# Performance work log

Hardware: AMD Instinct MI355X
Metric: run time of the kernel (lower is better)

## Reference

```python
import jax, jax.numpy as jnp
import numpy as np

B, V, E, H, L = 1024, 50257, 512, 512, 2


def setup_inputs() -> dict:
    key = jax.random.key(0)
    ks = jax.random.split(key, 12)
    s = 1.0 / np.sqrt(H)
    inp = {
        "x": jax.random.randint(ks[0], (B,), 0, V),
        "hidden": jnp.zeros((2 * L, B, H), jnp.float32),
        "embed": jax.random.normal(ks[1], (V, E), jnp.float32) * 0.02,
        # layer 0: input size E; layer 1: input size 2H (bidirectional concat)
        "Wih0": jax.random.uniform(ks[2], (2, 3 * H, E), jnp.float32, -s, s),
        "Whh0": jax.random.uniform(ks[3], (2, 3 * H, H), jnp.float32, -s, s),
        "bih0": jax.random.uniform(ks[4], (2, 3 * H), jnp.float32, -s, s),
        "bhh0": jax.random.uniform(ks[5], (2, 3 * H), jnp.float32, -s, s),
        "Wih1": jax.random.uniform(ks[6], (2, 3 * H, 2 * H), jnp.float32, -s, s),
        "Whh1": jax.random.uniform(ks[7], (2, 3 * H, H), jnp.float32, -s, s),
        "bih1": jax.random.uniform(ks[8], (2, 3 * H), jnp.float32, -s, s),
        "bhh1": jax.random.uniform(ks[9], (2, 3 * H), jnp.float32, -s, s),
        "Wproj": jax.random.uniform(ks[10], (V, E), jnp.float32, -1.0 / np.sqrt(E), 1.0 / np.sqrt(E)),
        "bproj": jax.random.uniform(ks[11], (V,), jnp.float32, -1.0 / np.sqrt(E), 1.0 / np.sqrt(E)),
    }
    return inp


def _gru_cell(x, h, Wih, Whh, bih, bhh):
    # PyTorch GRU cell: gates ordered (r, z, n)
    gi = x @ Wih.T + bih            # [B, 3H]
    gh = h @ Whh.T + bhh            # [B, 3H]
    ir, iz, inn = jnp.split(gi, 3, axis=-1)
    hr, hz, hn = jnp.split(gh, 3, axis=-1)
    r = jax.nn.sigmoid(ir + hr)
    z = jax.nn.sigmoid(iz + hz)
    n = jnp.tanh(inn + r * hn)
    return (1.0 - z) * n + z * h


def reference(x, hidden, embed, Wih0, Whh0, bih0, bhh0, Wih1, Whh1, bih1, bhh1, Wproj, bproj):
    inp = embed[x]                  # [B, E] embedding lookup; seq_len == 1
    layer_params = [(Wih0, Whh0, bih0, bhh0), (Wih1, Whh1, bih1, bhh1)]
    new_h = []
    for l, (Wih, Whh, bih, bhh) in enumerate(layer_params):
        # single timestep: fwd and bwd directions each do one cell step on the same input
        hf = _gru_cell(inp, hidden[2 * l],     Wih[0], Whh[0], bih[0], bhh[0])
        hb = _gru_cell(inp, hidden[2 * l + 1], Wih[1], Whh[1], bih[1], bhh[1])
        new_h += [hf, hb]
        inp = jnp.concatenate([hf, hb], axis=-1)   # [B, 2H]
    # x[:, :, hidden_dim:] -> backward-direction output of top layer, then transpose(0,1)
    out = hb[:, None, :]                            # [B, 1, H]
    logits = out @ Wproj.T + bproj                  # [B, 1, V]
    probs = jax.nn.softmax(logits, axis=-1)
    return probs, jnp.stack(new_h, axis=0)          # ([B,1,V], [2L, B, H])
```

## Files before the change

kernel.cpp:

```cpp
#include <hip/hip_runtime.h>


#define Bsz 1024
#define Hs  512
#define Vv  50257
#define VP  50304
#define NG  1536
#define NPB 393

typedef __bf16 bf16x8 __attribute__((ext_vector_type(8)));
typedef float  floatx4 __attribute__((ext_vector_type(4)));

__device__ __forceinline__ unsigned short f2bf(float f) {
  unsigned int u = __builtin_bit_cast(unsigned int, f);
  u += 0x7fffu + ((u >> 16) & 1u);
  return (unsigned short)(u >> 16);
}

__device__ __forceinline__ float bf2f(unsigned short u) {
  unsigned int x = (unsigned int)u << 16;
  return __builtin_bit_cast(float, x);
}

__device__ __forceinline__ void cvt4(const float* src, unsigned short* dst) {
  float4 f = *(const float4*)src;
  unsigned int lo = (unsigned int)f2bf(f.x) | ((unsigned int)f2bf(f.y) << 16);
  unsigned int hi = (unsigned int)f2bf(f.z) | ((unsigned int)f2bf(f.w) << 16);
  *(uint2*)dst = make_uint2(lo, hi);
}

__device__ __forceinline__ void g2lds16(const void* g, void* l) {
  unsigned long long gv = (unsigned long long)g;
  unsigned int lv = (unsigned int)(unsigned long long)l;
  __builtin_amdgcn_global_load_lds(
      (const __attribute__((address_space(1))) unsigned int*)gv,
      (__attribute__((address_space(3))) unsigned int*)lv,
      16, 0, 0);
}

__device__ __forceinline__ void compute_step(const unsigned short* Acur, const unsigned short* Bcur,
                                             floatx4 (&acc)[4][4], int wr, int wc, int g, int r16) {
#pragma unroll
  for (int ks = 0; ks < 2; ++ks) {
    bf16x8 a[4], b[4];
#pragma unroll
    for (int i = 0; i < 4; ++i) {
      int rowA = wr * 64 + i * 16 + r16;
      int ca = (ks * 4 + g) ^ (rowA & 7);
      a[i] = *(const bf16x8*)((const char*)Acur + rowA * 128 + ca * 16);
      int rowB = wc * 64 + i * 16 + r16;
      int cb = (ks * 4 + g) ^ (rowB & 7);
      b[i] = *(const bf16x8*)((const char*)Bcur + rowB * 128 + cb * 16);
    }
#pragma unroll
    for (int i = 0; i < 4; ++i)
#pragma unroll
      for (int j = 0; j < 4; ++j)
        acc[i][j] = __builtin_amdgcn_mfma_f32_16x16x32_bf16(a[i], b[j], acc[i][j], 0, 0, 0);
  }
}

__device__ __forceinline__ void gemm_core8(const unsigned short* A, const unsigned short* Bw, int K,
                                           int mt, int nt,
                                           unsigned short* Alds, unsigned short* Blds,
                                           floatx4 (&acc)[4][4]) {
  const int tid = threadIdx.x;
  const int w = tid >> 6, l = tid & 63;
  const int wr = w >> 1, wc = w & 1;
  const int g = l >> 4, r16 = l & 15;
  floatx4 zero = {0.f, 0.f, 0.f, 0.f};
#pragma unroll
  for (int i = 0; i < 4; ++i)
#pragma unroll
    for (int j = 0; j < 4; ++j) acc[i][j] = zero;

  const int nsteps = K >> 6;
  for (int kt = 0; kt < nsteps; ++kt) {
    __syncthreads();
#pragma unroll
    for (int i = 0; i < 4; ++i) {
      int chunk = w * 4 + i;
      int t16 = chunk * 64 + l;
      int row = t16 >> 3, c = t16 & 7;
      int sc = c ^ (row & 7);
      g2lds16(A + (size_t)(mt * 256 + row) * K + kt * 64 + sc * 8, (char*)Alds + chunk * 1024);
    }
#pragma unroll
    for (int i = 0; i < 2; ++i) {
      int chunk = w * 2 + i;
      int t16 = chunk * 64 + l;
      int row = t16 >> 3, c = t16 & 7;
      int sc = c ^ (row & 7);
      g2lds16(Bw + (size_t)(nt * 128 + row) * K + kt * 64 + sc * 8, (char*)Blds + chunk * 1024);
    }
    __syncthreads();
    compute_step(Alds, Blds, acc, wr, wc, g, r16);
  }
}

__device__ __forceinline__ void gemm_coreBf32(const unsigned short* A, const float* Bw, int K,
                                              int mt, int nt, int maxrowB,
                                              unsigned short* Alds, unsigned short* Blds,
                                              floatx4 (&acc)[4][4]) {
  const int tid = threadIdx.x;
  const int w = tid >> 6, l = tid & 63;
  const int wr = w >> 1, wc = w & 1;
  const int g = l >> 4, r16 = l & 15;
  floatx4 zero = {0.f, 0.f, 0.f, 0.f};
#pragma unroll
  for (int i = 0; i < 4; ++i)
#pragma unroll
    for (int j = 0; j < 4; ++j) acc[i][j] = zero;

  int brow[2], bsc[2];
#pragma unroll
  for (int i = 0; i < 2; ++i) {
    int chunk = w * 2 + i;
    int t16 = chunk * 64 + l;
    brow[i] = t16 >> 3;
    bsc[i] = (t16 & 7) ^ (brow[i] & 7);
  }
  int brg[2];
#pragma unroll
  for (int i = 0; i < 2; ++i) {
    int rg = nt * 128 + brow[i];
    brg[i] = (rg > maxrowB) ? maxrowB : rg;
  }

  const int nsteps = K >> 6;
  for (int kt = 0; kt < nsteps; ++kt) {
    __syncthreads();
    float4 rb[2][2];
#pragma unroll
    for (int i = 0; i < 2; ++i) {
      const float* src = Bw + (size_t)brg[i] * K + kt * 64 + bsc[i] * 8;
      rb[i][0] = *(const float4*)src;
      rb[i][1] = *(const float4*)(src + 4);
    }
#pragma unroll
    for (int i = 0; i < 4; ++i) {
      int chunk = w * 4 + i;
      int t16 = chunk * 64 + l;
      int row = t16 >> 3, c = t16 & 7;
      int sc = c ^ (row & 7);
      g2lds16(A + (size_t)(mt * 256 + row) * K + kt * 64 + sc * 8, (char*)Alds + chunk * 1024);
    }
#pragma unroll
    for (int i = 0; i < 2; ++i) {
      uint4 p;
      p.x = (unsigned int)f2bf(rb[i][0].x) | ((unsigned int)f2bf(rb[i][0].y) << 16);
      p.y = (unsigned int)f2bf(rb[i][0].z) | ((unsigned int)f2bf(rb[i][0].w) << 16);
      p.z = (unsigned int)f2bf(rb[i][1].x) | ((unsigned int)f2bf(rb[i][1].y) << 16);
      p.w = (unsigned int)f2bf(rb[i][1].z) | ((unsigned int)f2bf(rb[i][1].w) << 16);
      *(uint4*)((char*)Blds + (w * 2 + i) * 1024 + l * 16) = p;
    }
    __syncthreads();
    compute_step(Alds, Blds, acc, wr, wc, g, r16);
  }
}

struct GemmDesc {
  const unsigned short* A[4];
  const unsigned short* Bw[4];
  const float* bias[4];
  float* C[4];
  int K[4];
};

__global__ __launch_bounds__(512, 4) void gemm_gru_batch(GemmDesc d) {
  __shared__ alignas(16) unsigned short Alds[256 * 64];
  __shared__ alignas(16) unsigned short Blds[128 * 64];
  const int z = blockIdx.z;
  floatx4 acc[4][4];
  gemm_core8(d.A[z], d.Bw[z], d.K[z], blockIdx.y, blockIdx.x, Alds, Blds, acc);
  const float* bias = d.bias[z];
  float* C = d.C[z];
  const int tid = threadIdx.x, w = tid >> 6, l = tid & 63;
  const int wr = w >> 1, wc = w & 1, g = l >> 4, r16 = l & 15;
#pragma unroll
  for (int i = 0; i < 4; ++i)
#pragma unroll
    for (int j = 0; j < 4; ++j) {
      int col = blockIdx.x * 128 + wc * 64 + j * 16 + r16;
      float bc = bias[col];
#pragma unroll
      for (int q = 0; q < 4; ++q) {
        int row = blockIdx.y * 256 + wr * 64 + i * 16 + g * 4 + q;
        C[(size_t)row * NG + col] = acc[i][j][q] + bc;
      }
    }
}

template <int MODE>
__global__ __launch_bounds__(512, 4) void gemm_proj(const unsigned short* A, const float* Bw,
                                                    const float* biasp, unsigned short* stash,
                                                    float* probs, float* partial, const float* inv) {
  __shared__ alignas(16) unsigned short Alds[256 * 64];
  __shared__ alignas(16) unsigned short Blds[128 * 64];
  __shared__ float rowpart[256];
  const int tid = threadIdx.x;
  if (MODE != 2 && tid < 256) rowpart[tid] = 0.f;
  int orig = blockIdx.x;
  int xcd = orig & 7, slot = orig >> 3;
  int wgid = (xcd < 4 ? xcd * 197 : 788 + (xcd - 4) * 196) + slot;
  int mt = wgid & 3, nt = wgid >> 2;
  floatx4 acc[4][4];
  gemm_coreBf32(A, Bw, 512, mt, nt, Vv - 1, Alds, Blds, acc);
  const int w = tid >> 6, l = tid & 63;
  const int wr = w >> 1, wc = w & 1, g = l >> 4, r16 = l & 15;
  float bcol[4];
#pragma unroll
  for (int j = 0; j < 4; ++j) bcol[j] = biasp[nt * 128 + wc * 64 + j * 16 + r16];
#pragma unroll
  for (int i = 0; i < 4; ++i)
#pragma unroll
    for (int q = 0; q < 4; ++q) {
      int rowl = wr * 64 + i * 16 + g * 4 + q;
      int grow = mt * 256 + rowl;
      float rinv = (MODE == 2) ? inv[grow] : 0.f;
      float s = 0.f;
#pragma unroll
      for (int j = 0; j < 4; ++j) {
        int col = nt * 128 + wc * 64 + j * 16 + r16;
        float v = __expf(acc[i][j][q] + bcol[j]);
        if (MODE == 0) stash[(size_t)grow * VP + col] = f2bf(v);
        if (MODE == 2) { if (col < Vv) probs[(size_t)grow * Vv + col] = v * rinv; }
        s += v;
      }
      if (MODE != 2) {
        s += __shfl_xor(s, 1); s += __shfl_xor(s, 2);
        s += __shfl_xor(s, 4); s += __shfl_xor(s, 8);
        if (r16 == 0) atomicAdd(&rowpart[rowl], s);
      }
    }
  if (MODE != 2) {
    __syncthreads();
    if (tid < 256) partial[(size_t)(mt * 256 + tid) * NPB + nt] = rowpart[tid];
  }
}

__global__ __launch_bounds__(256) void gru_gates(const float* Cbuf, const float* hidden,
                                                 float* out_newh, unsigned short* bf_out, int layer) {
  int idx = blockIdx.x * 256 + threadIdx.x;
  int j = idx & 511;
  int b = (idx >> 9) & 1023;
  int d = idx >> 19;
  const float* GI = Cbuf + (size_t)d * Bsz * NG;
  const float* GH = Cbuf + (size_t)(2 + d) * Bsz * NG;
  size_t base = (size_t)b * NG + j;
  float ir = GI[base], iz = GI[base + 512], inn = GI[base + 1024];
  float hr = GH[base], hz = GH[base + 512], hn = GH[base + 1024];
  float r = 1.f / (1.f + __expf(-(ir + hr)));
  float z = 1.f / (1.f + __expf(-(iz + hz)));
  float n = tanhf(inn + r * hn);
  size_t hoff = (size_t)(2 * layer + d) * (Bsz * Hs) + (size_t)b * Hs + j;
  float hprev = hidden[hoff];
  float h = (1.f - z) * n + z * hprev;
  out_newh[hoff] = h;
  if (layer == 0) {
    bf_out[(size_t)b * 1024 + d * 512 + j] = f2bf(h);
  } else if (d == 1) {
    bf_out[(size_t)b * 512 + j] = f2bf(h);
  }
}

__global__ void convert_small(const float* Wih0, const float* Whh0, const float* Wih1,
                              const float* Whh1, const float* hidden, const float* bproj,
                              unsigned short* wih0b, unsigned short* whh0b, unsigned short* wih1b,
                              unsigned short* whh1b, unsigned short* hbf, float* bprojp) {
  long long idx = ((long long)blockIdx.x * 256 + threadIdx.x) * 4;
  if (idx < 1572864) { cvt4(Wih0 + idx, wih0b + idx); return; }
  idx -= 1572864;
  if (idx < 1572864) { cvt4(Whh0 + idx, whh0b + idx); return; }
  idx -= 1572864;
  if (idx < 3145728) { cvt4(Wih1 + idx, wih1b + idx); return; }
  idx -= 3145728;
  if (idx < 1572864) { cvt4(Whh1 + idx, whh1b + idx); return; }
  idx -= 1572864;
  if (idx < 2097152) { cvt4(hidden + idx, hbf + idx); return; }
  idx -= 2097152;
  if (idx < VP) {
    float4 v;
    v.x = (idx + 0 < Vv) ? bproj[idx + 0] : -1e30f;
    v.y = (idx + 1 < Vv) ? bproj[idx + 1] : -1e30f;
    v.z = (idx + 2 < Vv) ? bproj[idx + 2] : -1e30f;
    v.w = (idx + 3 < Vv) ? bproj[idx + 3] : -1e30f;
    *(float4*)(bprojp + idx) = v;
  }
}

__global__ void gather_embed(const int* x, const float* embed, unsigned short* xe) {
  int b = blockIdx.x, t = threadIdx.x;
  int tok = x[b];
  float2 v = *(const float2*)(embed + (size_t)tok * 512 + t * 2);
  unsigned int o = ((unsigned int)f2bf(v.y) << 16) | f2bf(v.x);
  *(unsigned int*)((unsigned short*)xe + (size_t)b * 512 + t * 2) = o;
}

__global__ void rowsum_inv(const float* partial, float* inv) {
  int row = blockIdx.x, tid = threadIdx.x;
  float s = 0.f;
  for (int c = tid; c < NPB; c += 128) s += partial[(size_t)row * NPB + c];
  __shared__ float tmp[128];
  tmp[tid] = s;
  __syncthreads();
  for (int off = 64; off > 0; off >>= 1) {
    if (tid < off) tmp[tid] += tmp[tid + off];
    __syncthreads();
  }
  if (tid == 0) inv[row] = 1.0f / tmp[0];
}

__global__ __launch_bounds__(256) void scale_expand(const unsigned short* stash, const float* inv,
                                                    float* probs) {
  const unsigned int nquad = 12865792u;
  const unsigned int step = gridDim.x * 256u;
  for (unsigned int f = blockIdx.x * 256u + threadIdx.x; f < nquad; f += step) {
    unsigned int e0 = f * 4u;
    unsigned int row = e0 / (unsigned int)Vv;
    int col = (int)(e0 - row * (unsigned int)Vv);
    float4 o;
    if (col + 4 <= Vv) {
      float s = inv[row];
      const unsigned short* sp = stash + (size_t)row * VP + col;
      if ((col & 1) == 0) {
        unsigned int u0 = *(const unsigned int*)sp;
        unsigned int u1 = *(const unsigned int*)(sp + 2);
        o.x = bf2f((unsigned short)u0) * s;
        o.y = bf2f((unsigned short)(u0 >> 16)) * s;
        o.z = bf2f((unsigned short)u1) * s;
        o.w = bf2f((unsigned short)(u1 >> 16)) * s;
      } else {
        o.x = bf2f(sp[0]) * s; o.y = bf2f(sp[1]) * s;
        o.z = bf2f(sp[2]) * s; o.w = bf2f(sp[3]) * s;
      }
    } else {
      float vals[4];
#pragma unroll
      for (int k = 0; k < 4; ++k) {
        unsigned int e = e0 + k;
        unsigned int rk = e / (unsigned int)Vv;
        int ck = (int)(e - rk * (unsigned int)Vv);
        vals[k] = bf2f(stash[(size_t)rk * VP + ck]) * inv[rk];
      }
      o.x = vals[0]; o.y = vals[1]; o.z = vals[2]; o.w = vals[3];
    }
    *(float4*)(probs + e0) = o;
  }
}

extern "C" void kernel_launch(void* const* d_in, const int* in_sizes, int n_in,
                              void* d_out, int out_size, void* d_ws, size_t ws_size,
                              hipStream_t stream) {
  const int*   x      = (const int*)d_in[0];
  const float* hidden = (const float*)d_in[1];
  const float* embed  = (const float*)d_in[2];
  const float* Wih0   = (const float*)d_in[3];
  const float* Whh0   = (const float*)d_in[4];
  const float* bih0   = (const float*)d_in[5];
  const float* bhh0   = (const float*)d_in[6];
  const float* Wih1   = (const float*)d_in[7];
  const float* Whh1   = (const float*)d_in[8];
  const float* bih1   = (const float*)d_in[9];
  const float* bhh1   = (const float*)d_in[10];
  const float* Wproj  = (const float*)d_in[11];
  const float* bproj  = (const float*)d_in[12];
  float* out = (float*)d_out;

  char* ws = (char*)d_ws;
  unsigned short* wih0b  = (unsigned short*)(ws);
  unsigned short* whh0b  = (unsigned short*)(ws + 3145728);
  unsigned short* wih1b  = (unsigned short*)(ws + 6291456);
  unsigned short* whh1b  = (unsigned short*)(ws + 12582912);
  unsigned short* hbf    = (unsigned short*)(ws + 15728640);
  float*          bprojp = (float*)(ws + 19922944);
  unsigned short* xe     = (unsigned short*)(ws + 20124160);
  unsigned short* inp1   = (unsigned short*)(ws + 21172736);
  unsigned short* hb1    = (unsigned short*)(ws + 23269888);
  float*          Cbuf   = (float*)(ws + 24318464);
  float*          partial= (float*)(ws + 49484288);
  float*          inv    = (float*)(ws + 51094016);
  unsigned short* stash  = (unsigned short*)(ws + 51098112);
  const size_t NEED_STASH = 51098112ull + (size_t)Bsz * VP * 2ull;

  float* out_newh = out + 51463168ll;

  convert_small<<<9778, 256, 0, stream>>>(Wih0, Whh0, Wih1, Whh1, hidden, bproj,
                                          wih0b, whh0b, wih1b, whh1b, hbf, bprojp);
  gather_embed<<<1024, 256, 0, stream>>>(x, embed, xe);

  GemmDesc d0;
  d0.A[0] = xe;  d0.A[1] = xe;
  d0.A[2] = hbf; d0.A[3] = hbf + 524288;
  d0.Bw[0] = wih0b; d0.Bw[1] = wih0b + 786432;
  d0.Bw[2] = whh0b; d0.Bw[3] = whh0b + 786432;
  d0.bias[0] = bih0; d0.bias[1] = bih0 + 1536;
  d0.bias[2] = bhh0; d0.bias[3] = bhh0 + 1536;
  d0.C[0] = Cbuf;             d0.C[1] = Cbuf + 1572864;
  d0.C[2] = Cbuf + 2*1572864; d0.C[3] = Cbuf + 3*1572864;
  d0.K[0] = d0.K[1] = d0.K[2] = d0.K[3] = 512;
  gemm_gru_batch<<<dim3(12, 4, 4), 512, 0, stream>>>(d0);
  gru_gates<<<4096, 256, 0, stream>>>(Cbuf, hidden, out_newh, inp1, 0);

  GemmDesc d1;
  d1.A[0] = inp1; d1.A[1] = inp1;
  d1.A[2] = hbf + 2*524288; d1.A[3] = hbf + 3*524288;
  d1.Bw[0] = wih1b; d1.Bw[1] = wih1b + 1572864;
  d1.Bw[2] = whh1b; d1.Bw[3] = whh1b + 786432;
  d1.bias[0] = bih1; d1.bias[1] = bih1 + 1536;
  d1.bias[2] = bhh1; d1.bias[3] = bhh1 + 1536;
  d1.C[0] = Cbuf;             d1.C[1] = Cbuf + 1572864;
  d1.C[2] = Cbuf + 2*1572864; d1.C[3] = Cbuf + 3*1572864;
  d1.K[0] = d1.K[1] = 1024; d1.K[2] = d1.K[3] = 512;
  gemm_gru_batch<<<dim3(12, 4, 4), 512, 0, stream>>>(d1);
  gru_gates<<<4096, 256, 0, stream>>>(Cbuf, hidden, out_newh, hb1, 1);

  if (ws_size >= NEED_STASH) {
    gemm_proj<0><<<1572, 512, 0, stream>>>(hb1, Wproj, bprojp, stash, out, partial, inv);
    rowsum_inv<<<1024, 128, 0, stream>>>(partial, inv);
    scale_expand<<<8192, 256, 0, stream>>>(stash, inv, out);
  } else {
    gemm_proj<1><<<1572, 512, 0, stream>>>(hb1, Wproj, bprojp, stash, out, partial, inv);
    rowsum_inv<<<1024, 128, 0, stream>>>(partial, inv);
    gemm_proj<2><<<1572, 512, 0, stream>>>(hb1, Wproj, bprojp, stash, out, partial, inv);
  }
}
```

Baseline: 252.4 us.

## Pre-convert Wproj to bf16 and use pipelined 256x256 projection GEMM

Adds a conversion of Wproj to padded bf16 in the setup kernel and replaces the projection GEMM with a 256x256-tile kernel that double-buffers A and B tiles via direct global-to-LDS loads, interleaving MFMA phases with staging. This removes repeated fp32 loads and per-tile bf16 conversion of Wproj and halves the number of partial-sum columns. It costs an extra full pass over Wproj per call, a larger workspace requirement, and lower occupancy from the bigger tiles.

```diff
diff --git a/kernel.cpp b/kernel.cpp
--- a/kernel.cpp
+++ b/kernel.cpp
@@ -4,9 +4,10 @@
 #define Bsz 1024
 #define Hs  512
 #define Vv  50257
-#define VP  50304
+#define VP2 50432
 #define NG  1536
-#define NPB 393
+#define NPB2 197
+#define NPBF 393
 
 typedef __bf16 bf16x8 __attribute__((ext_vector_type(8)));
 typedef float  floatx4 __attribute__((ext_vector_type(4)));
@@ -36,6 +37,130 @@
       (const __attribute__((address_space(1))) unsigned int*)gv,
       (__attribute__((address_space(3))) unsigned int*)lv,
       16, 0, 0);
+}
+
+__device__ __forceinline__ void stage_half512(const unsigned short* src, long long rowBase,
+                                              unsigned short* tile, int half, int kOff,
+                                              int w, int l) {
+#pragma unroll
+  for (int i = 0; i < 2; ++i) {
+    int t16 = (i * 8 + w) * 64 + l;
+    int row = t16 >> 3, c = t16 & 7;
+    int sc = c ^ (row & 7);
+    const unsigned short* g = src + (rowBase + half * 128 + row) * 512ll + kOff + sc * 8;
+    g2lds16(g, (char*)tile + half * 16384 + (i * 8 + w) * 1024 + l * 16);
+  }
+}
+
+#define PHASEQ(Q)                                                                           \
+  do {                                                                                      \
+    bf16x8 afr[2][2];                                                                       \
+    _Pragma("unroll") for (int mm = 0; mm < 2; ++mm)                                        \
+    _Pragma("unroll") for (int ks = 0; ks < 2; ++ks) {                                      \
+      int rowA = wr * 128 + (2 * (Q) + mm) * 16 + r16;                                      \
+      int slot = (ks * 4 + g) ^ (rowA & 7);                                                 \
+      afr[mm][ks] = *(const bf16x8*)((const char*)Ac + rowA * 128 + slot * 16);             \
+    }                                                                                       \
+    __builtin_amdgcn_s_barrier();                                                           \
+    __builtin_amdgcn_s_setprio(1);                                                          \
+    _Pragma("unroll") for (int ks = 0; ks < 2; ++ks)                                        \
+    _Pragma("unroll") for (int mm = 0; mm < 2; ++mm)                                        \
+    _Pragma("unroll") for (int nf = 0; nf < 4; ++nf)                                        \
+      acc[2 * (Q) + mm][nf] = __builtin_amdgcn_mfma_f32_16x16x32_bf16(                      \
+          afr[mm][ks], bfr[nf][ks], acc[2 * (Q) + mm][nf], 0, 0, 0);                        \
+    __builtin_amdgcn_s_setprio(0);                                                          \
+    __builtin_amdgcn_s_barrier();                                                           \
+  } while (0)
+
+__global__ __launch_bounds__(512, 2) void gemm_proj8(const unsigned short* A, const unsigned short* Bw,
+                                                     const float* biasp, unsigned short* stash,
+                                                     float* partial) {
+  __shared__ alignas(16) unsigned short Ab[2][16384];
+  __shared__ alignas(16) unsigned short Bb[2][16384];
+  __shared__ float rowpart[256][4];
+  const int tid = threadIdx.x;
+  const int w = tid >> 6, l = tid & 63;
+  const int wr = w >> 2, wc = w & 3;
+  const int g = l >> 4, r16 = l & 15;
+  int orig = blockIdx.x;
+  int xcd = orig & 7, slot = orig >> 3;
+  int wgid = (xcd < 4 ? xcd * 99 : 396 + (xcd - 4) * 98) + slot;
+  int mt = wgid & 3, nt = wgid >> 2;
+
+  floatx4 acc[8][4];
+  floatx4 zero = {0.f, 0.f, 0.f, 0.f};
+#pragma unroll
+  for (int i = 0; i < 8; ++i)
+#pragma unroll
+    for (int j = 0; j < 4; ++j) acc[i][j] = zero;
+
+  const long long mrb = (long long)mt * 256;
+  const long long nrb = (long long)nt * 256;
+
+  stage_half512(Bw, nrb, Bb[0], 0, 0, w, l);
+  stage_half512(Bw, nrb, Bb[0], 1, 0, w, l);
+  stage_half512(A,  mrb, Ab[0], 0, 0, w, l);
+  stage_half512(A,  mrb, Ab[0], 1, 0, w, l);
+  stage_half512(Bw, nrb, Bb[1], 0, 64, w, l);
+  stage_half512(Bw, nrb, Bb[1], 1, 64, w, l);
+  asm volatile("s_waitcnt vmcnt(4)" ::: "memory");
+  __builtin_amdgcn_s_barrier();
+
+#pragma unroll
+  for (int t = 0; t < 8; ++t) {
+    const int c = t & 1;
+    const unsigned short* Ac = Ab[c];
+    const unsigned short* Bc = Bb[c];
+    if (t > 0) {
+      if (t < 7) asm volatile("s_waitcnt vmcnt(4)" ::: "memory");
+      else       asm volatile("s_waitcnt vmcnt(0)" ::: "memory");
+      __builtin_amdgcn_s_barrier();
+    }
+    if (t + 1 < 8) stage_half512(A, mrb, Ab[c ^ 1], 0, (t + 1) * 64, w, l);
+    bf16x8 bfr[4][2];
+#pragma unroll
+    for (int nf = 0; nf < 4; ++nf)
+#pragma unroll
+      for (int ks = 0; ks < 2; ++ks) {
+        int rowB = wc * 64 + nf * 16 + r16;
+        int slotb = (ks * 4 + g) ^ (rowB & 7);
+        bfr[nf][ks] = *(const bf16x8*)((const char*)Bc + rowB * 128 + slotb * 16);
+      }
+    PHASEQ(0);
+    if (t + 1 < 8) stage_half512(A, mrb, Ab[c ^ 1], 1, (t + 1) * 64, w, l);
+    PHASEQ(1);
+    if (t + 2 < 8) stage_half512(Bw, nrb, Bb[c], 0, (t + 2) * 64, w, l);
+    PHASEQ(2);
+    if (t + 2 < 8) stage_half512(Bw, nrb, Bb[c], 1, (t + 2) * 64, w, l);
+    PHASEQ(3);
+  }
+
+  float bcol[4];
+#pragma unroll
+  for (int nf = 0; nf < 4; ++nf) bcol[nf] = biasp[nt * 256 + wc * 64 + nf * 16 + r16];
+#pragma unroll
+  for (int mf = 0; mf < 8; ++mf)
+#pragma unroll
+    for (int qq = 0; qq < 4; ++qq) {
+      int rowl = wr * 128 + mf * 16 + g * 4 + qq;
+      long long grow = mt * 256 + rowl;
+      float s = 0.f;
+#pragma unroll
+      for (int nf = 0; nf < 4; ++nf) {
+        int col = nt * 256 + wc * 64 + nf * 16 + r16;
+        float v = __expf(acc[mf][nf][qq] + bcol[nf]);
+        stash[grow * VP2 + col] = f2bf(v);
+        s += v;
+      }
+      s += __shfl_xor(s, 1); s += __shfl_xor(s, 2);
+      s += __shfl_xor(s, 4); s += __shfl_xor(s, 8);
+      if (r16 == 0) rowpart[rowl][wc] = s;
+    }
+  __syncthreads();
+  if (tid < 256) {
+    float t4 = (rowpart[tid][0] + rowpart[tid][1]) + (rowpart[tid][2] + rowpart[tid][3]);
+    partial[(size_t)(mt * 256 + tid) * NPB2 + nt] = t4;
+  }
 }
 
 __device__ __forceinline__ void compute_step(const unsigned short* Acur, const unsigned short* Bcur,
@@ -92,67 +217,6 @@
       int row = t16 >> 3, c = t16 & 7;
       int sc = c ^ (row & 7);
       g2lds16(Bw + (size_t)(nt * 128 + row) * K + kt * 64 + sc * 8, (char*)Blds + chunk * 1024);
-    }
-    __syncthreads();
-    compute_step(Alds, Blds, acc, wr, wc, g, r16);
-  }
-}
-
-__device__ __forceinline__ void gemm_coreBf32(const unsigned short* A, const float* Bw, int K,
-                                              int mt, int nt, int maxrowB,
-                                              unsigned short* Alds, unsigned short* Blds,
-                                              floatx4 (&acc)[4][4]) {
-  const int tid = threadIdx.x;
-  const int w = tid >> 6, l = tid & 63;
-  const int wr = w >> 1, wc = w & 1;
-  const int g = l >> 4, r16 = l & 15;
-  floatx4 zero = {0.f, 0.f, 0.f, 0.f};
-#pragma unroll
-  for (int i = 0; i < 4; ++i)
-#pragma unroll
-    for (int j = 0; j < 4; ++j) acc[i][j] = zero;
-
-  int brow[2], bsc[2];
-#pragma unroll
-  for (int i = 0; i < 2; ++i) {
-    int chunk = w * 2 + i;
-    int t16 = chunk * 64 + l;
-    brow[i] = t16 >> 3;
-    bsc[i] = (t16 & 7) ^ (brow[i] & 7);
-  }
-  int brg[2];
-#pragma unroll
-  for (int i = 0; i < 2; ++i) {
-    int rg = nt * 128 + brow[i];
-    brg[i] = (rg > maxrowB) ? maxrowB : rg;
-  }
-
-  const int nsteps = K >> 6;
-  for (int kt = 0; kt < nsteps; ++kt) {
-    __syncthreads();
-    float4 rb[2][2];
-#pragma unroll
-    for (int i = 0; i < 2; ++i) {
-      const float* src = Bw + (size_t)brg[i] * K + kt * 64 + bsc[i] * 8;
-      rb[i][0] = *(const float4*)src;
-      rb[i][1] = *(const float4*)(src + 4);
-    }
-#pragma unroll
-    for (int i = 0; i < 4; ++i) {
-      int chunk = w * 4 + i;
-      int t16 = chunk * 64 + l;
-      int row = t16 >> 3, c = t16 & 7;
-      int sc = c ^ (row & 7);
-      g2lds16(A + (size_t)(mt * 256 + row) * K + kt * 64 + sc * 8, (char*)Alds + chunk * 1024);
-    }
-#pragma unroll
-    for (int i = 0; i < 2; ++i) {
-      uint4 p;
-      p.x = (unsigned int)f2bf(rb[i][0].x) | ((unsigned int)f2bf(rb[i][0].y) << 16);
-      p.y = (unsigned int)f2bf(rb[i][0].z) | ((unsigned int)f2bf(rb[i][0].w) << 16);
-      p.z = (unsigned int)f2bf(rb[i][1].x) | ((unsigned int)f2bf(rb[i][1].y) << 16);
-      p.w = (unsigned int)f2bf(rb[i][1].z) | ((unsigned int)f2bf(rb[i][1].w) << 16);
-      *(uint4*)((char*)Blds + (w * 2 + i) * 1024 + l * 16) = p;
     }
     __syncthreads();
     compute_step(Alds, Blds, acc, wr, wc, g, r16);
@@ -191,10 +255,65 @@
     }
 }
 
+__device__ __forceinline__ void gemm_coreBf32(const unsigned short* A, const float* Bw, int K,
+                                              int mt, int nt, int maxrowB,
+                                              unsigned short* Alds, unsigned short* Blds,
+                                              floatx4 (&acc)[4][4]) {
+  const int tid = threadIdx.x;
+  const int w = tid >> 6, l = tid & 63;
+  const int wr = w >> 1, wc = w & 1;
+  const int g = l >> 4, r16 = l & 15;
+  floatx4 zero = {0.f, 0.f, 0.f, 0.f};
+#pragma unroll
+  for (int i = 0; i < 4; ++i)
+#pragma unroll
+    for (int j = 0; j < 4; ++j) acc[i][j] = zero;
+  int brow[2], bsc[2], brg[2];
+#pragma unroll
+  for (int i = 0; i < 2; ++i) {
+    int chunk = w * 2 + i;
+    int t16 = chunk * 64 + l;
+    brow[i] = t16 >> 3;
+    bsc[i] = (t16 & 7) ^ (brow[i] & 7);
+    int rg = nt * 128 + brow[i];
+    brg[i] = (rg > maxrowB) ? maxrowB : rg;
+  }
+  const int nsteps = K >> 6;
+  for (int kt = 0; kt < nsteps; ++kt) {
+    __syncthreads();
+    float4 rb[2][2];
+#pragma unroll
+    for (int i = 0; i < 2; ++i) {
+      const float* src = Bw + (size_t)brg[i] * K + kt * 64 + bsc[i] * 8;
+      rb[i][0] = *(const float4*)src;
+      rb[i][1] = *(const float4*)(src + 4);
+    }
+#pragma unroll
+    for (int i = 0; i < 4; ++i) {
+      int chunk = w * 4 + i;
+      int t16 = chunk * 64 + l;
+      int row = t16 >> 3, c = t16 & 7;
+      int sc = c ^ (row & 7);
+      g2lds16(A + (size_t)(mt * 256 + row) * K + kt * 64 + sc * 8, (char*)Alds + chunk * 1024);
+    }
+#pragma unroll
+    for (int i = 0; i < 2; ++i) {
+      uint4 p;
+      p.x = (unsigned int)f2bf(rb[i][0].x) | ((unsigned int)f2bf(rb[i][0].y) << 16);
+      p.y = (unsigned int)f2bf(rb[i][0].z) | ((unsigned int)f2bf(rb[i][0].w) << 16);
+      p.z = (unsigned int)f2bf(rb[i][1].x) | ((unsigned int)f2bf(rb[i][1].y) << 16);
+      p.w = (unsigned int)f2bf(rb[i][1].z) | ((unsigned int)f2bf(rb[i][1].w) << 16);
+      *(uint4*)((char*)Blds + (w * 2 + i) * 1024 + l * 16) = p;
+    }
+    __syncthreads();
+    compute_step(Alds, Blds, acc, wr, wc, g, r16);
+  }
+}
+
 template <int MODE>
-__global__ __launch_bounds__(512, 4) void gemm_proj(const unsigned short* A, const float* Bw,
-                                                    const float* biasp, unsigned short* stash,
-                                                    float* probs, float* partial, const float* inv) {
+__global__ __launch_bounds__(512, 4) void gemm_proj_fb(const unsigned short* A, const float* Bw,
+                                                       const float* biasp, float* probs,
+                                                       float* partial, const float* inv) {
   __shared__ alignas(16) unsigned short Alds[256 * 64];
   __shared__ alignas(16) unsigned short Blds[128 * 64];
   __shared__ float rowpart[256];
@@ -223,7 +342,6 @@
       for (int j = 0; j < 4; ++j) {
         int col = nt * 128 + wc * 64 + j * 16 + r16;
         float v = __expf(acc[i][j][q] + bcol[j]);
-        if (MODE == 0) stash[(size_t)grow * VP + col] = f2bf(v);
         if (MODE == 2) { if (col < Vv) probs[(size_t)grow * Vv + col] = v * rinv; }
         s += v;
       }
@@ -235,7 +353,7 @@
     }
   if (MODE != 2) {
     __syncthreads();
-    if (tid < 256) partial[(size_t)(mt * 256 + tid) * NPB + nt] = rowpart[tid];
+    if (tid < 256) partial[(size_t)(mt * 256 + tid) * NPBF + nt] = rowpart[tid];
   }
 }
 
@@ -264,10 +382,11 @@
   }
 }
 
-__global__ void convert_small(const float* Wih0, const float* Whh0, const float* Wih1,
-                              const float* Whh1, const float* hidden, const float* bproj,
-                              unsigned short* wih0b, unsigned short* whh0b, unsigned short* wih1b,
-                              unsigned short* whh1b, unsigned short* hbf, float* bprojp) {
+__global__ void convert_all(const float* Wih0, const float* Whh0, const float* Wih1, const float* Whh1,
+                            const float* hidden, const float* Wproj, const float* bproj,
+                            unsigned short* wih0b, unsigned short* whh0b, unsigned short* wih1b,
+                            unsigned short* whh1b, unsigned short* hbf, unsigned short* wprojb,
+                            float* bprojp) {
   long long idx = ((long long)blockIdx.x * 256 + threadIdx.x) * 4;
   if (idx < 1572864) { cvt4(Wih0 + idx, wih0b + idx); return; }
   idx -= 1572864;
@@ -279,7 +398,14 @@
   idx -= 1572864;
   if (idx < 2097152) { cvt4(hidden + idx, hbf + idx); return; }
   idx -= 2097152;
-  if (idx < VP) {
+  if (idx < 25821184) {
+    long long row = idx >> 9, col = idx & 511;
+    if (row < Vv) cvt4(Wproj + row * 512 + col, wprojb + idx);
+    else *(uint2*)(wprojb + idx) = make_uint2(0u, 0u);
+    return;
+  }
+  idx -= 25821184;
+  if (idx < VP2) {
     float4 v;
     v.x = (idx + 0 < Vv) ? bproj[idx + 0] : -1e30f;
     v.y = (idx + 1 < Vv) ? bproj[idx + 1] : -1e30f;
@@ -297,10 +423,10 @@
   *(unsigned int*)((unsigned short*)xe + (size_t)b * 512 + t * 2) = o;
 }
 
-__global__ void rowsum_inv(const float* partial, float* inv) {
+__global__ void rowsum_inv(const float* partial, float* inv, int npb) {
   int row = blockIdx.x, tid = threadIdx.x;
   float s = 0.f;
-  for (int c = tid; c < NPB; c += 128) s += partial[(size_t)row * NPB + c];
+  for (int c = tid; c < npb; c += 128) s += partial[(size_t)row * npb + c];
   __shared__ float tmp[128];
   tmp[tid] = s;
   __syncthreads();
@@ -322,7 +448,7 @@
     float4 o;
     if (col + 4 <= Vv) {
       float s = inv[row];
-      const unsigned short* sp = stash + (size_t)row * VP + col;
+      const unsigned short* sp = stash + (size_t)row * VP2 + col;
       if ((col & 1) == 0) {
         unsigned int u0 = *(const unsigned int*)sp;
         unsigned int u1 = *(const unsigned int*)(sp + 2);
@@ -341,7 +467,7 @@
         unsigned int e = e0 + k;
         unsigned int rk = e / (unsigned int)Vv;
         int ck = (int)(e - rk * (unsigned int)Vv);
-        vals[k] = bf2f(stash[(size_t)rk * VP + ck]) * inv[rk];
+        vals[k] = bf2f(stash[(size_t)rk * VP2 + ck]) * inv[rk];
       }
       o.x = vals[0]; o.y = vals[1]; o.z = vals[2]; o.w = vals[3];
     }
@@ -374,19 +500,20 @@
   unsigned short* whh1b  = (unsigned short*)(ws + 12582912);
   unsigned short* hbf    = (unsigned short*)(ws + 15728640);
   float*          bprojp = (float*)(ws + 19922944);
-  unsigned short* xe     = (unsigned short*)(ws + 20124160);
-  unsigned short* inp1   = (unsigned short*)(ws + 21172736);
-  unsigned short* hb1    = (unsigned short*)(ws + 23269888);
-  float*          Cbuf   = (float*)(ws + 24318464);
-  float*          partial= (float*)(ws + 49484288);
-  float*          inv    = (float*)(ws + 51094016);
-  unsigned short* stash  = (unsigned short*)(ws + 51098112);
-  const size_t NEED_STASH = 51098112ull + (size_t)Bsz * VP * 2ull;
+  unsigned short* xe     = (unsigned short*)(ws + 20124672);
+  unsigned short* inp1   = (unsigned short*)(ws + 21173248);
+  unsigned short* hb1    = (unsigned short*)(ws + 23270400);
+  unsigned short* wprojb = (unsigned short*)(ws + 24318976);
+  float*          partial= (float*)(ws + 75961344);
+  float*          inv    = (float*)(ws + 77571072);
+  float*          Cbuf   = (float*)(ws + 77575168);
+  unsigned short* stash  = (unsigned short*)(ws + 77575168);
+  const size_t NEED_STASH = 77575168ull + (size_t)Bsz * VP2 * 2ull;
 
   float* out_newh = out + 51463168ll;
 
-  convert_small<<<9778, 256, 0, stream>>>(Wih0, Whh0, Wih1, Whh1, hidden, bproj,
-                                          wih0b, whh0b, wih1b, whh1b, hbf, bprojp);
+  convert_all<<<34994, 256, 0, stream>>>(Wih0, Whh0, Wih1, Whh1, hidden, Wproj, bproj,
+                                         wih0b, whh0b, wih1b, whh1b, hbf, wprojb, bprojp);
   gather_embed<<<1024, 256, 0, stream>>>(x, embed, xe);
 
   GemmDesc d0;
@@ -416,12 +543,12 @@
   gru_gates<<<4096, 256, 0, stream>>>(Cbuf, hidden, out_newh, hb1, 1);
 
   if (ws_size >= NEED_STASH) {
-    gemm_proj<0><<<1572, 512, 0, stream>>>(hb1, Wproj, bprojp, stash, out, partial, inv);
-    rowsum_inv<<<1024, 128, 0, stream>>>(partial, inv);
+    gemm_proj8<<<788, 512, 0, stream>>>(hb1, wprojb, bprojp, stash, partial);
+    rowsum_inv<<<1024, 128, 0, stream>>>(partial, inv, NPB2);
     scale_expand<<<8192, 256, 0, stream>>>(stash, inv, out);
   } else {
-    gemm_proj<1><<<1572, 512, 0, stream>>>(hb1, Wproj, bprojp, stash, out, partial, inv);
-    rowsum_inv<<<1024, 128, 0, stream>>>(partial, inv);
-    gemm_proj<2><<<1572, 512, 0, stream>>>(hb1, Wproj, bprojp, stash, out, partial, inv);
-  }
-}
+    gemm_proj_fb<1><<<1572, 512, 0, stream>>>(hb1, Wproj, bprojp, out, partial, inv);
+    rowsum_inv<<<1024, 128, 0, stream>>>(partial, inv, NPBF);
+    gemm_proj_fb<2><<<1572, 512, 0, stream>>>(hb1, Wproj, bprojp, out, partial, inv);
+  }
+}
```

After: 251.1 us. No clear change (-0.5%).
